# Kernel tuning notes

Measured on AMD Instinct MI355X. Metric: run time of the kernel, lower is better.

## Reference

```python
import jax, jax.numpy as jnp
import numpy as np

B, S, D = 2, 2048, 1024
H = 16
HD = D // H  # 64


def _xavier(key, shape):
    fan_in, fan_out = shape[1], shape[0]
    a = jnp.sqrt(6.0 / (fan_in + fan_out))
    return jax.random.uniform(key, shape, jnp.float32, -a, a)


def setup_inputs() -> dict:
    key = jax.random.key(0)
    ks = jax.random.split(key, 7)
    xq = jax.random.normal(ks[0], (B, S, D), jnp.float32)
    xv = jax.random.normal(ks[1], (B, S, D), jnp.float32)
    xk = jax.random.normal(ks[2], (B, S, D), jnp.float32)
    Wq = _xavier(ks[3], (D, D)); bq = jnp.zeros((D,), jnp.float32)
    Wk = _xavier(ks[4], (D, D)); bk = jnp.zeros((D,), jnp.float32)
    Wv = _xavier(ks[5], (D, D)); bv = jnp.zeros((D,), jnp.float32)
    Wo = _xavier(ks[6], (D, D)); bo = jnp.zeros((D,), jnp.float32)
    return {"xq": xq, "xv": xv, "xk": xk,
            "Wq": Wq, "bq": bq, "Wk": Wk, "bk": bk,
            "Wv": Wv, "bv": bv, "Wo": Wo, "bo": bo}


def reference(xq, xv, xk, Wq, bq, Wk, bk, Wv, bv, Wo, bo):
    # Q/K/V projections (torch Linear: x @ W.T + b), split heads -> [B,H,S,HD]
    q = (xq @ Wq.T + bq).reshape(B, S, H, HD).transpose(0, 2, 1, 3)
    k = (xk @ Wk.T + bk).reshape(B, S, H, HD).transpose(0, 2, 1, 3)
    v = (xv @ Wv.T + bv).reshape(B, S, H, HD).transpose(0, 2, 1, 3)
    # scaled dot-product attention, no mask
    logits = jnp.einsum('bhqd,bhkd->bhqk', q, k) / jnp.sqrt(jnp.float32(HD))
    attn = jax.nn.softmax(logits, axis=-1)
    values = jnp.einsum('bhqk,bhkd->bhqd', attn, v)
    values = values.transpose(0, 2, 1, 3).reshape(B, S, D)
    return values @ Wo.T + bo
```

## Files before the change

### kernel.cpp

```cpp
#include <hip/hip_runtime.h>

typedef __bf16 bf16x8 __attribute__((ext_vector_type(8)));
typedef float f32x4 __attribute__((ext_vector_type(4)));
typedef __attribute__((address_space(1))) const unsigned char ga_t;
typedef __attribute__((address_space(3))) unsigned char la_t;

static __device__ __forceinline__ unsigned short f2b(float f) {
  union { float f; unsigned int i; } c; c.f = f;
  unsigned int r = c.i + 0x7FFFu + ((c.i >> 16) & 1u);
  return (unsigned short)(r >> 16);
}
static __device__ __forceinline__ unsigned int pack2(float a, float b) {
  return (unsigned int)f2b(a) | ((unsigned int)f2b(b) << 16);
}
static __device__ __forceinline__ int4 ld8f_cvt(const float* __restrict__ p) {
  float4 a = *(const float4*)p;
  float4 b = *(const float4*)(p + 4);
  unsigned short u[8];
  u[0] = f2b(a.x); u[1] = f2b(a.y); u[2] = f2b(a.z); u[3] = f2b(a.w);
  u[4] = f2b(b.x); u[5] = f2b(b.y); u[6] = f2b(b.z); u[7] = f2b(b.w);
  return *(int4*)u;
}
static __device__ __forceinline__ void glds16(const unsigned short* g, unsigned short* l) {
  __builtin_amdgcn_global_load_lds((ga_t*)g, (la_t*)l, 16, 0, 0);
}

__global__ __launch_bounds__(256)
void cvt_z(const float* __restrict__ s0, const float* __restrict__ s1,
           const float* __restrict__ s2, const float* __restrict__ s3,
           unsigned short* d0, unsigned short* d1,
           unsigned short* d2, unsigned short* d3, int n8) {
  const int z = blockIdx.y;
  const float* s = z == 0 ? s0 : z == 1 ? s1 : z == 2 ? s2 : s3;
  unsigned short* d = z == 0 ? d0 : z == 1 ? d1 : z == 2 ? d2 : d3;
  int idx = blockIdx.x * 256 + threadIdx.x;
  if (idx < n8) *(int4*)(d + (size_t)idx * 8) = ld8f_cvt(s + (size_t)idx * 8);
}

static __device__ __forceinline__ void gemm_core(
    const unsigned short* __restrict__ A, const unsigned short* __restrict__ W,
    unsigned short* sA, unsigned short* sB, f32x4 acc[4][4],
    int K, int m0, int n0) {
  const int tid = threadIdx.x;
  const int wave = tid >> 6, lane = tid & 63, quad = lane >> 4, l16 = lane & 15;
  const int wrow = (wave >> 1) * 64, wcol = (wave & 1) * 64;
  const int r = tid >> 2, c8 = (tid & 3) * 8;

  const unsigned short* gA0 = A + (size_t)(m0 + r) * K + c8;
  const unsigned short* gA1 = gA0 + (size_t)64 * K;
  const unsigned short* gB0 = W + (size_t)(n0 + r) * K + c8;
  const unsigned short* gB1 = gB0 + (size_t)64 * K;
  unsigned short* lA0 = sA + tid * 8;
  unsigned short* lA1 = lA0 + 2048;
  unsigned short* lB0 = sB + tid * 8;
  unsigned short* lB1 = lB0 + 2048;

  for (int k0 = 0; k0 < K; k0 += 32) {
    __syncthreads();
    glds16(gA0 + k0, lA0);
    glds16(gA1 + k0, lA1);
    glds16(gB0 + k0, lB0);
    glds16(gB1 + k0, lB1);
    __syncthreads();

    bf16x8 af[4], bfv[4];
#pragma unroll
    for (int i = 0; i < 4; ++i)
      af[i] = *(const bf16x8*)(&sA[(wrow + i * 16 + l16) * 32 + quad * 8]);
#pragma unroll
    for (int j = 0; j < 4; ++j)
      bfv[j] = *(const bf16x8*)(&sB[(wcol + j * 16 + l16) * 32 + quad * 8]);
#pragma unroll
    for (int i = 0; i < 4; ++i)
#pragma unroll
      for (int j = 0; j < 4; ++j)
        acc[i][j] = __builtin_amdgcn_mfma_f32_16x16x32_bf16(af[i], bfv[j], acc[i][j], 0, 0, 0);
  }
}

__global__ __launch_bounds__(256, 3)
void gemm_qkv(const unsigned short* __restrict__ A0p, const unsigned short* __restrict__ A1p,
              const unsigned short* __restrict__ A2p,
              const unsigned short* __restrict__ W0p, const unsigned short* __restrict__ W1p,
              const unsigned short* __restrict__ W2p,
              const float* __restrict__ b0p, const float* __restrict__ b1p,
              const float* __restrict__ b2p,
              unsigned short* __restrict__ C0p, unsigned short* __restrict__ C1p,
              unsigned short* __restrict__ C2p,
              int M, int N, int K, int zbase) {
  __shared__ __align__(16) unsigned short smem[8192];
  const int z = blockIdx.z + zbase;
  const unsigned short* A = z == 0 ? A0p : z == 1 ? A1p : A2p;
  const unsigned short* W = z == 0 ? W0p : z == 1 ? W1p : W2p;
  const float* bias = z == 0 ? b0p : z == 1 ? b1p : b2p;

  const int tid = threadIdx.x;
  const int wave = tid >> 6, lane = tid & 63, quad = lane >> 4, l16 = lane & 15;
  const int m0 = blockIdx.x * 128, n0 = blockIdx.y * 128;
  const int wrow = (wave >> 1) * 64, wcol = (wave & 1) * 64;

  f32x4 acc[4][4];
#pragma unroll
  for (int i = 0; i < 4; ++i)
#pragma unroll
    for (int j = 0; j < 4; ++j) acc[i][j] = (f32x4){0.f, 0.f, 0.f, 0.f};

  gemm_core(A, W, smem, smem + 4096, acc, K, m0, n0);

  if (z < 2) {
    unsigned short* C = z == 0 ? C0p : C1p;
#pragma unroll
    for (int j = 0; j < 4; ++j) {
      const int col = n0 + wcol + j * 16 + l16;
      const float bv = bias[col];
#pragma unroll
      for (int i = 0; i < 4; ++i)
#pragma unroll
        for (int r = 0; r < 4; ++r) {
          const int row = m0 + wrow + i * 16 + quad * 4 + r;
          C[(size_t)row * N + col] = f2b(acc[i][j][r] + bv);
        }
    }
  } else {
    __syncthreads();
    unsigned short* sT = smem + wave * 1152;
#pragma unroll
    for (int j = 0; j < 4; ++j) {
      const float bv = bias[n0 + wcol + j * 16 + l16];
#pragma unroll
      for (int i = 0; i < 4; ++i) {
        uint2 pk;
        pk.x = pack2(acc[i][j][0] + bv, acc[i][j][1] + bv);
        pk.y = pack2(acc[i][j][2] + bv, acc[i][j][3] + bv);
        *(uint2*)(&sT[l16 * 72 + i * 16 + quad * 4]) = pk;
      }
#pragma unroll
      for (int t = 0; t < 2; ++t) {
        const int nl = lane >> 2;
        const int colh = (lane & 3) * 8 + t * 32;
        int4 v = *(const int4*)(&sT[nl * 72 + colh]);
        *(int4*)(&C2p[(size_t)(n0 + wcol + j * 16 + nl) * M + m0 + wrow + colh]) = v;
      }
    }
  }
}

__global__ __launch_bounds__(256, 3)
void gemm_out(const unsigned short* __restrict__ A, const unsigned short* __restrict__ W,
              const float* __restrict__ bias, float* __restrict__ C,
              int M, int N, int K) {
  __shared__ __align__(16) unsigned short smem[8192];
  const int tid = threadIdx.x;
  const int wave = tid >> 6, lane = tid & 63, quad = lane >> 4, l16 = lane & 15;
  const int m0 = blockIdx.x * 128, n0 = blockIdx.y * 128;
  const int wrow = (wave >> 1) * 64, wcol = (wave & 1) * 64;

  f32x4 acc[4][4];
#pragma unroll
  for (int i = 0; i < 4; ++i)
#pragma unroll
    for (int j = 0; j < 4; ++j) acc[i][j] = (f32x4){0.f, 0.f, 0.f, 0.f};

  gemm_core(A, W, smem, smem + 4096, acc, K, m0, n0);

#pragma unroll
  for (int j = 0; j < 4; ++j) {
    const int col = n0 + wcol + j * 16 + l16;
    const float bv = bias[col];
#pragma unroll
    for (int i = 0; i < 4; ++i)
#pragma unroll
      for (int r = 0; r < 4; ++r) {
        const int row = m0 + wrow + i * 16 + quad * 4 + r;
        C[(size_t)row * N + col] = acc[i][j][r] + bv;
      }
  }
}

#define SEQ 2048
#define DMODEL 1024

__global__ __launch_bounds__(256, 2)
void attn_fused(const unsigned short* __restrict__ Q,
                const unsigned short* __restrict__ Km,
                const unsigned short* __restrict__ Vt,
                unsigned short* __restrict__ O) {
  __shared__ __align__(16) unsigned short sU[128 * 72];
  __shared__ __align__(16) unsigned short sK[64 * 72];
  __shared__ __align__(16) unsigned short sVt[64 * 72];

  const int tid = threadIdx.x;
  const int wave = tid >> 6, lane = tid & 63, quad = lane >> 4, l16 = lane & 15;
  const int qt = blockIdx.x;
  const int bh = blockIdx.y;
  const int b = bh >> 4, h = bh & 15;
  const size_t qrow0 = (size_t)b * SEQ + qt * 128;
  const size_t kvrow0 = (size_t)b * SEQ;
  const int hcol = h * 64;
  const int bofs = b * SEQ;

#pragma unroll
  for (int i = 0; i < 4; ++i) {
    const int idx = tid + i * 256;
    const int r = idx >> 3, c = (idx & 7) * 8;
    *(int4*)(&sU[r * 72 + c]) = *(const int4*)(&Q[(qrow0 + r) * DMODEL + hcol + c]);
  }
  __syncthreads();

  const int qw = wave * 32;
  bf16x8 qa[2][2];
#pragma unroll
  for (int qi = 0; qi < 2; ++qi)
#pragma unroll
    for (int ks = 0; ks < 2; ++ks)
      qa[qi][ks] = *(const bf16x8*)(&sU[(qw + qi * 16 + l16) * 72 + ks * 32 + quad * 8]);

  unsigned short* sP = sU + wave * (32 * 72);

  f32x4 acc[2][4];
#pragma unroll
  for (int qi = 0; qi < 2; ++qi)
#pragma unroll
    for (int hg = 0; hg < 4; ++hg) acc[qi][hg] = (f32x4){0.f, 0.f, 0.f, 0.f};
  float lsum[2] = {0.f, 0.f};

  const float SCL = 0.18033688011112042f;
  const int sr = tid >> 3, sc = (tid & 7) * 8;

  for (int kt = 0; kt < SEQ; kt += 64) {
    __syncthreads();
    {
      const int idx2 = tid + 256;
      const int r2 = idx2 >> 3, c2 = (idx2 & 7) * 8;
      *(int4*)(&sK[sr * 72 + sc]) = *(const int4*)(&Km[(kvrow0 + kt + sr) * DMODEL + hcol + sc]);
      *(int4*)(&sK[r2 * 72 + c2]) = *(const int4*)(&Km[(kvrow0 + kt + r2) * DMODEL + hcol + c2]);
      *(int4*)(&sVt[sr * 72 + sc]) = *(const int4*)(&Vt[(size_t)(hcol + sr) * 4096 + bofs + kt + sc]);
      *(int4*)(&sVt[r2 * 72 + c2]) = *(const int4*)(&Vt[(size_t)(hcol + r2) * 4096 + bofs + kt + c2]);
    }
    __syncthreads();

    f32x4 s[2][4];
#pragma unroll
    for (int qi = 0; qi < 2; ++qi)
#pragma unroll
      for (int kg = 0; kg < 4; ++kg) s[qi][kg] = (f32x4){0.f, 0.f, 0.f, 0.f};
#pragma unroll
    for (int kg = 0; kg < 4; ++kg) {
      bf16x8 kb0 = *(const bf16x8*)(&sK[(kg * 16 + l16) * 72 + quad * 8]);
      bf16x8 kb1 = *(const bf16x8*)(&sK[(kg * 16 + l16) * 72 + 32 + quad * 8]);
#pragma unroll
      for (int qi = 0; qi < 2; ++qi) {
        s[qi][kg] = __builtin_amdgcn_mfma_f32_16x16x32_bf16(kb0, qa[qi][0], s[qi][kg], 0, 0, 0);
        s[qi][kg] = __builtin_amdgcn_mfma_f32_16x16x32_bf16(kb1, qa[qi][1], s[qi][kg], 0, 0, 0);
      }
    }

#pragma unroll
    for (int qi = 0; qi < 2; ++qi)
#pragma unroll
      for (int kg = 0; kg < 4; ++kg) {
        float p0 = __builtin_amdgcn_exp2f(s[qi][kg][0] * SCL);
        float p1 = __builtin_amdgcn_exp2f(s[qi][kg][1] * SCL);
        float p2 = __builtin_amdgcn_exp2f(s[qi][kg][2] * SCL);
        float p3 = __builtin_amdgcn_exp2f(s[qi][kg][3] * SCL);
        lsum[qi] += (p0 + p1) + (p2 + p3);
        uint2 pk; pk.x = pack2(p0, p1); pk.y = pack2(p2, p3);
        *(uint2*)(&sP[(qi * 16 + l16) * 72 + kg * 16 + quad * 4]) = pk;
      }

#pragma unroll
    for (int ks = 0; ks < 2; ++ks) {
      bf16x8 pa[2], vb[4];
#pragma unroll
      for (int qi = 0; qi < 2; ++qi)
        pa[qi] = *(const bf16x8*)(&sP[(qi * 16 + l16) * 72 + ks * 32 + quad * 8]);
#pragma unroll
      for (int hg = 0; hg < 4; ++hg)
        vb[hg] = *(const bf16x8*)(&sVt[(hg * 16 + l16) * 72 + ks * 32 + quad * 8]);
#pragma unroll
      for (int qi = 0; qi < 2; ++qi)
#pragma unroll
        for (int hg = 0; hg < 4; ++hg)
          acc[qi][hg] = __builtin_amdgcn_mfma_f32_16x16x32_bf16(pa[qi], vb[hg], acc[qi][hg], 0, 0, 0);
    }
  }

#pragma unroll
  for (int qi = 0; qi < 2; ++qi) {
    float v = lsum[qi];
    v += __shfl_xor(v, 16, 64);
    v += __shfl_xor(v, 32, 64);
    lsum[qi] = v;
  }
  float linv[2][4];
#pragma unroll
  for (int qi = 0; qi < 2; ++qi)
#pragma unroll
    for (int r = 0; r < 4; ++r)
      linv[qi][r] = 1.0f / __shfl(lsum[qi], quad * 4 + r, 64);

#pragma unroll
  for (int qi = 0; qi < 2; ++qi)
#pragma unroll
    for (int hg = 0; hg < 4; ++hg)
#pragma unroll
      for (int r = 0; r < 4; ++r) {
        const size_t row = qrow0 + qw + qi * 16 + quad * 4 + r;
        O[row * DMODEL + hcol + hg * 16 + l16] = f2b(acc[qi][hg][r] * linv[qi][r]);
      }
}

extern "C" void kernel_launch(void* const* d_in, const int* in_sizes, int n_in,
                              void* d_out, int out_size, void* d_ws, size_t ws_size,
                              hipStream_t stream) {
  const float* xq = (const float*)d_in[0];
  const float* xv = (const float*)d_in[1];
  const float* xk = (const float*)d_in[2];
  const float* Wq = (const float*)d_in[3];
  const float* bq = (const float*)d_in[4];
  const float* Wk = (const float*)d_in[5];
  const float* bk = (const float*)d_in[6];
  const float* Wv = (const float*)d_in[7];
  const float* bv = (const float*)d_in[8];
  const float* Wo = (const float*)d_in[9];
  const float* bo = (const float*)d_in[10];
  float* out = (float*)d_out;

  const int S = 2048, D = 1024, M = 4096;
  const size_t MD = (size_t)M * D, DD = (size_t)D * D;
  unsigned short* P = (unsigned short*)d_ws;
  dim3 bb(256);
  dim3 gg(M / 128, D / 128);

  const size_t need = (3 * MD + 4 * DD + 3 * MD) * 2;
  if (ws_size >= need) {
    unsigned short* Ab = P;
    unsigned short* Wb = Ab + 3 * MD;
    unsigned short* Qw = Wb + 4 * DD;
    unsigned short* Kw = Qw + MD;
    unsigned short* Vtw = Kw + MD;
    unsigned short* Ao = Ab;

    cvt_z<<<dim3((int)(MD / 8 / 256), 3), bb, 0, stream>>>(
        xq, xk, xv, xq, Ab, Ab + MD, Ab + 2 * MD, Ab, (int)(MD / 8));
    cvt_z<<<dim3((int)(DD / 8 / 256), 4), bb, 0, stream>>>(
        Wq, Wk, Wv, Wo, Wb, Wb + DD, Wb + 2 * DD, Wb + 3 * DD, (int)(DD / 8));
    gemm_qkv<<<dim3(M / 128, D / 128, 3), bb, 0, stream>>>(
        Ab, Ab + MD, Ab + 2 * MD, Wb, Wb + DD, Wb + 2 * DD,
        bq, bk, bv, Qw, Kw, Vtw, M, D, D, 0);
    attn_fused<<<dim3(S / 128, 32), bb, 0, stream>>>(Qw, Kw, Vtw, Ao);
    gemm_out<<<gg, bb, 0, stream>>>(Ao, Wb + 3 * DD, bo, out, M, D, D);
  } else {
    unsigned short* Ab = P;
    unsigned short* Wb = Ab + MD;
    unsigned short* Qw = Wb + DD;
    unsigned short* Kw = Qw + MD;
    unsigned short* Vtw = Kw + MD;
    unsigned short* Ao = Ab;
    const int an = (int)(MD / 8), wn = (int)(DD / 8);

    cvt_z<<<dim3(an / 256, 1), bb, 0, stream>>>(xq, xq, xq, xq, Ab, Ab, Ab, Ab, an);
    cvt_z<<<dim3(wn / 256, 1), bb, 0, stream>>>(Wq, Wq, Wq, Wq, Wb, Wb, Wb, Wb, wn);
    gemm_qkv<<<dim3(M / 128, D / 128, 1), bb, 0, stream>>>(
        Ab, Ab, Ab, Wb, Wb, Wb, bq, bq, bq, Qw, Qw, Qw, M, D, D, 0);

    cvt_z<<<dim3(an / 256, 1), bb, 0, stream>>>(xk, xk, xk, xk, Ab, Ab, Ab, Ab, an);
    cvt_z<<<dim3(wn / 256, 1), bb, 0, stream>>>(Wk, Wk, Wk, Wk, Wb, Wb, Wb, Wb, wn);
    gemm_qkv<<<dim3(M / 128, D / 128, 1), bb, 0, stream>>>(
        Ab, Ab, Ab, Wb, Wb, Wb, bk, bk, bk, Kw, Kw, Kw, M, D, D, 0);

    cvt_z<<<dim3(an / 256, 1), bb, 0, stream>>>(xv, xv, xv, xv, Ab, Ab, Ab, Ab, an);
    cvt_z<<<dim3(wn / 256, 1), bb, 0, stream>>>(Wv, Wv, Wv, Wv, Wb, Wb, Wb, Wb, wn);
    gemm_qkv<<<dim3(M / 128, D / 128, 1), bb, 0, stream>>>(
        Ab, Ab, Ab, Wb, Wb, Wb, bv, bv, bv, Vtw, Vtw, Vtw, M, D, D, 2);

    attn_fused<<<dim3(S / 128, 32), bb, 0, stream>>>(Qw, Kw, Vtw, Ao);

    cvt_z<<<dim3(wn / 256, 1), bb, 0, stream>>>(Wo, Wo, Wo, Wo, Wb, Wb, Wb, Wb, wn);
    gemm_out<<<gg, bb, 0, stream>>>(Ao, Wb, bo, out, M, D, D);
  }
}
```

Baseline: 253.3 us.

## Double-buffer K/V tiles with async global-to-LDS loads in attention kernel

Replaces the synchronous register-staged K/V tile loads with global_load_lds DMA into two alternating LDS buffers. The next tile is prefetched while the current one is computed, which cuts one barrier per iteration. Tiles are stored in MFMA-fragment order so LDS reads are contiguous per lane, and Q fragments are now loaded straight from global memory into registers. This relies on the barrier waiting for outstanding LDS DMA before reads, and it issues one redundant prefetch on the last iteration.

```diff
diff --git a/kernel.cpp b/kernel.cpp
--- a/kernel.cpp
+++ b/kernel.cpp
@@ -185,9 +185,9 @@
                 const unsigned short* __restrict__ Km,
                 const unsigned short* __restrict__ Vt,
                 unsigned short* __restrict__ O) {
-  __shared__ __align__(16) unsigned short sU[128 * 72];
-  __shared__ __align__(16) unsigned short sK[64 * 72];
-  __shared__ __align__(16) unsigned short sVt[64 * 72];
+  __shared__ __align__(16) unsigned short sK[2][4096];
+  __shared__ __align__(16) unsigned short sVt[2][4096];
+  __shared__ __align__(16) unsigned short sPb[4][2304];
 
   const int tid = threadIdx.x;
   const int wave = tid >> 6, lane = tid & 63, quad = lane >> 4, l16 = lane & 15;
@@ -198,24 +198,18 @@
   const size_t kvrow0 = (size_t)b * SEQ;
   const int hcol = h * 64;
   const int bofs = b * SEQ;
-
-#pragma unroll
-  for (int i = 0; i < 4; ++i) {
-    const int idx = tid + i * 256;
-    const int r = idx >> 3, c = (idx & 7) * 8;
-    *(int4*)(&sU[r * 72 + c]) = *(const int4*)(&Q[(qrow0 + r) * DMODEL + hcol + c]);
-  }
-  __syncthreads();
-
   const int qw = wave * 32;
+
   bf16x8 qa[2][2];
 #pragma unroll
   for (int qi = 0; qi < 2; ++qi)
 #pragma unroll
-    for (int ks = 0; ks < 2; ++ks)
-      qa[qi][ks] = *(const bf16x8*)(&sU[(qw + qi * 16 + l16) * 72 + ks * 32 + quad * 8]);
-
-  unsigned short* sP = sU + wave * (32 * 72);
+    for (int ks = 0; ks < 2; ++ks) {
+      int4 v = *(const int4*)(&Q[(qrow0 + qw + qi * 16 + l16) * DMODEL + hcol + ks * 32 + quad * 8]);
+      qa[qi][ks] = *(bf16x8*)&v;
+    }
+
+  unsigned short* sP = sPb[wave];
 
   f32x4 acc[2][4];
 #pragma unroll
@@ -225,19 +219,30 @@
   float lsum[2] = {0.f, 0.f};
 
   const float SCL = 0.18033688011112042f;
-  const int sr = tid >> 3, sc = (tid & 7) * 8;
+
+  const unsigned short* gK0 = Km + (kvrow0 + wave * 16 + l16) * DMODEL + hcol + quad * 8;
+  const unsigned short* gV0 = Vt + (size_t)(hcol + wave * 16 + l16) * 4096 + bofs + quad * 8;
+  unsigned short* lK0 = &sK[0][wave * 1024 + lane * 8];
+  unsigned short* lV0 = &sVt[0][wave * 1024 + lane * 8];
+
+#pragma unroll
+  for (int half = 0; half < 2; ++half) {
+    glds16(gK0 + half * 32, lK0 + half * 512);
+    glds16(gV0 + half * 32, lV0 + half * 512);
+  }
 
   for (int kt = 0; kt < SEQ; kt += 64) {
+    const int pb = (kt >> 6) & 1;
     __syncthreads();
-    {
-      const int idx2 = tid + 256;
-      const int r2 = idx2 >> 3, c2 = (idx2 & 7) * 8;
-      *(int4*)(&sK[sr * 72 + sc]) = *(const int4*)(&Km[(kvrow0 + kt + sr) * DMODEL + hcol + sc]);
-      *(int4*)(&sK[r2 * 72 + c2]) = *(const int4*)(&Km[(kvrow0 + kt + r2) * DMODEL + hcol + c2]);
-      *(int4*)(&sVt[sr * 72 + sc]) = *(const int4*)(&Vt[(size_t)(hcol + sr) * 4096 + bofs + kt + sc]);
-      *(int4*)(&sVt[r2 * 72 + c2]) = *(const int4*)(&Vt[(size_t)(hcol + r2) * 4096 + bofs + kt + c2]);
-    }
-    __syncthreads();
+
+    const int ktn = (kt + 64 < SEQ) ? kt + 64 : kt;
+    unsigned short* lKn = lK0 + (pb ^ 1) * 4096;
+    unsigned short* lVn = lV0 + (pb ^ 1) * 4096;
+#pragma unroll
+    for (int half = 0; half < 2; ++half) {
+      glds16(gK0 + (size_t)ktn * DMODEL + half * 32, lKn + half * 512);
+      glds16(gV0 + ktn + half * 32, lVn + half * 512);
+    }
 
     f32x4 s[2][4];
 #pragma unroll
@@ -246,8 +251,8 @@
       for (int kg = 0; kg < 4; ++kg) s[qi][kg] = (f32x4){0.f, 0.f, 0.f, 0.f};
 #pragma unroll
     for (int kg = 0; kg < 4; ++kg) {
-      bf16x8 kb0 = *(const bf16x8*)(&sK[(kg * 16 + l16) * 72 + quad * 8]);
-      bf16x8 kb1 = *(const bf16x8*)(&sK[(kg * 16 + l16) * 72 + 32 + quad * 8]);
+      bf16x8 kb0 = *(const bf16x8*)(&sK[pb][(kg * 2 + 0) * 512 + lane * 8]);
+      bf16x8 kb1 = *(const bf16x8*)(&sK[pb][(kg * 2 + 1) * 512 + lane * 8]);
 #pragma unroll
       for (int qi = 0; qi < 2; ++qi) {
         s[qi][kg] = __builtin_amdgcn_mfma_f32_16x16x32_bf16(kb0, qa[qi][0], s[qi][kg], 0, 0, 0);
@@ -276,7 +281,7 @@
         pa[qi] = *(const bf16x8*)(&sP[(qi * 16 + l16) * 72 + ks * 32 + quad * 8]);
 #pragma unroll
       for (int hg = 0; hg < 4; ++hg)
-        vb[hg] = *(const bf16x8*)(&sVt[(hg * 16 + l16) * 72 + ks * 32 + quad * 8]);
+        vb[hg] = *(const bf16x8*)(&sVt[pb][(hg * 2 + ks) * 512 + lane * 8]);
 #pragma unroll
       for (int qi = 0; qi < 2; ++qi)
 #pragma unroll
```

Result: faster. 242.2 us (-4.4%).
